# Performance work log

Measured on AMD Instinct MI355X. Metric: run time of the kernel, lower is better.

The kernel has to match this reference:

```python
import jax, jax.numpy as jnp
import numpy as np

C, G = 128, 2000          # num_cells, total_genes
CE, GE, H = 64, 64, 256   # cell_embed_dim, gene_embed_dim, hidden_dim
F = CE + GE + 3           # FCGNN input: ctrl val + cell_embed + gene_embed + shift + num_cells


def setup_inputs() -> dict:
    key = jax.random.key(0)
    ks = jax.random.split(key, 13)
    s = 0.02
    return {
        "ctrl": jax.random.uniform(ks[0], (C, G), dtype=jnp.float32),
        "shift_vec": jax.random.normal(ks[1], (G,), dtype=jnp.float32),
        "gene_indices": jnp.arange(G, dtype=jnp.int32),
        # CellEmbedding params
        "ce_w1": jax.random.normal(ks[2], (G, H), dtype=jnp.float32) * s,
        "ce_b1": jnp.zeros((H,), dtype=jnp.float32),
        "ce_w2": jax.random.normal(ks[3], (H, CE), dtype=jnp.float32) * s,
        "ce_b2": jnp.zeros((CE,), dtype=jnp.float32),
        # gene embedding table
        "gene_table": jax.random.normal(ks[4], (G, GE), dtype=jnp.float32) * s,
        # FCGNN params
        "g_w1": jax.random.normal(ks[5], (F, H), dtype=jnp.float32) * s,
        "g_b1": jnp.zeros((H,), dtype=jnp.float32),
        "g_w2": jax.random.normal(ks[6], (2 * H, H), dtype=jnp.float32) * s,
        "g_b2": jnp.zeros((H,), dtype=jnp.float32),
        "g_w3": jax.random.normal(ks[7], (2 * H, 1), dtype=jnp.float32) * s,
        "g_b3": jnp.zeros((1,), dtype=jnp.float32),
    }


def reference(ctrl, shift_vec, gene_indices, ce_w1, ce_b1, ce_w2, ce_b2,
              gene_table, g_w1, g_b1, g_w2, g_b2, g_w3, g_b3):
    num_cells = ctrl.shape[0]
    num_genes = gene_indices.shape[0]

    # CellEmbedding: fc2(elu(fc1(ctrl)))  -> [C, CE]
    ce = jax.nn.elu(ctrl @ ce_w1 + ce_b1) @ ce_w2 + ce_b2

    ctrl_g = ctrl[:, gene_indices]           # [C, Gn]
    shift = shift_vec[gene_indices]          # [Gn]
    ge = gene_table[gene_indices]            # [Gn, GE]

    # Build [C, Gn, F] feature tensor (ctrl val, cell embed, gene embed, shift, num_cells)
    z = jnp.concatenate([
        ctrl_g[:, :, None],
        jnp.broadcast_to(ce[:, None, :], (num_cells, num_genes, ce.shape[1])),
        jnp.broadcast_to(ge[None, :, :], (num_cells, num_genes, ge.shape[1])),
        jnp.broadcast_to(shift[None, :, None], (num_cells, num_genes, 1)),
        jnp.full((num_cells, num_genes, 1), float(num_cells), dtype=ctrl.dtype),
    ], axis=2)

    # FCGNN applied per gene (vectorized over gene axis); pooling is mean over cells (axis 0)
    x = jax.nn.elu(z @ g_w1 + g_b1)                                   # [C, Gn, H]
    p = x.mean(axis=0)                                                # [Gn, H]
    x = jnp.concatenate([x, jnp.broadcast_to(p[None], x.shape)], -1) @ g_w2 + g_b2
    p = x.mean(axis=0)
    x = jax.nn.elu(jnp.concatenate([x, jnp.broadcast_to(p[None], x.shape)], -1)) @ g_w3 + g_b3
    out = x[..., 0]                                                   # [C, Gn]

    # softmax over cells (torch Softmax(dim=0) after transpose/squeeze)
    return jax.nn.softmax(out, axis=0)
```

## Files before the change

kernel.cpp:

```cpp
#include <hip/hip_runtime.h>
#include <math.h>

#define G_GENES 2000
#define C_CELLS 128
#define H_DIM   256
#define CE_DIM  64
#define LDAe    264

typedef __attribute__((ext_vector_type(8))) short short8;
typedef __attribute__((ext_vector_type(4))) float floatx4;

__device__ __forceinline__ float eluf(float x) {
    float e = __expf(x) - 1.0f;
    return x > 0.0f ? x : e;
}
__device__ __forceinline__ unsigned short f2bf(float v) {
    unsigned u = __float_as_uint(v);
    u += 0x7FFF + ((u >> 16) & 1);
    return (unsigned short)(u >> 16);
}
__device__ __forceinline__ float bf2f(unsigned short s) {
    return __uint_as_float(((unsigned)s) << 16);
}

__global__ __launch_bounds__(256) void k1a(
    const float* __restrict__ ctrl, const float* __restrict__ ce_w1,
    float* __restrict__ hidpart)
{
    __shared__ float crow[250];
    const int c  = blockIdx.x >> 3;
    const int kc = blockIdx.x & 7;
    const int t  = threadIdx.x;

    if (t < 250) crow[t] = ctrl[(size_t)c * G_GENES + kc * 250 + t];
    __syncthreads();

    float s0 = 0.f, s1 = 0.f;
    const float* w = ce_w1 + (size_t)(kc * 250) * H_DIM + t;
    #pragma unroll 5
    for (int k = 0; k < 250; k += 2) {
        s0 = fmaf(crow[k], w[(size_t)k * H_DIM], s0);
        s1 = fmaf(crow[k + 1], w[(size_t)(k + 1) * H_DIM], s1);
    }
    hidpart[((size_t)c * 8 + kc) * H_DIM + t] = s0 + s1;
}

__global__ __launch_bounds__(256) void k1b(
    const float* __restrict__ hidpart, const float* __restrict__ ce_b1,
    const float* __restrict__ ce_w2, const float* __restrict__ ce_b2,
    const float* __restrict__ g_w1, float* __restrict__ Atc)
{
    __shared__ float hid[H_DIM];
    __shared__ float cel[CE_DIM];
    const int c = blockIdx.x;
    const int t = threadIdx.x;

    float s = ce_b1[t];
    #pragma unroll
    for (int p = 0; p < 8; ++p) s += hidpart[((size_t)c * 8 + p) * H_DIM + t];
    hid[t] = eluf(s);
    __syncthreads();

    if (t < CE_DIM) {
        float q = ce_b2[t];
        #pragma unroll 8
        for (int h = 0; h < H_DIM; ++h) q = fmaf(hid[h], ce_w2[(size_t)h * CE_DIM + t], q);
        cel[t] = q;
    }
    __syncthreads();

    float a = 0.f;
    #pragma unroll 8
    for (int e = 0; e < CE_DIM; ++e) a = fmaf(cel[e], g_w1[(size_t)(1 + e) * H_DIM + t], a);
    Atc[(size_t)c * H_DIM + t] = a;
}

__global__ __launch_bounds__(256) void k_w2abt(
    const float* __restrict__ g_w2, unsigned short* __restrict__ w2abt)
{
    const int n = blockIdx.x;
    const int k = threadIdx.x;
    w2abt[(size_t)n * H_DIM + k] = f2bf(g_w2[(size_t)k * H_DIM + n]);
}

__global__ __launch_bounds__(512, 4) void k_main(
    const float* __restrict__ ctrl, const float* __restrict__ shiftv,
    const int* __restrict__ gidx, const float* __restrict__ gtab,
    const float* __restrict__ g_w1, const float* __restrict__ g_b1,
    const float* __restrict__ g_w2, const float* __restrict__ g_b2,
    const float* __restrict__ g_w3, const float* __restrict__ Atc,
    const unsigned short* __restrict__ w2abt, float* __restrict__ out)
{
    __shared__ __align__(16) unsigned short x1t[C_CELLS * LDAe];
    __shared__ float cc[C_CELLS];
    __shared__ float gt[CE_DIM];
    __shared__ __align__(16) float Bv[H_DIM];
    __shared__ __align__(16) float w1r0[H_DIM];
    __shared__ float w3v[H_DIM];
    __shared__ float pvec[H_DIM];
    __shared__ float qv[H_DIM];
    __shared__ float red2[C_CELLS * 5];
    __shared__ float wred[4];

    const int g = blockIdx.x;
    const int t = threadIdx.x;
    const int idx = gidx[g];

    if (t < C_CELLS) cc[t] = ctrl[(size_t)t * G_GENES + idx];
    else if (t < C_CELLS + CE_DIM) gt[t - C_CELLS] = gtab[(size_t)idx * CE_DIM + (t - C_CELLS)];
    __syncthreads();

    if (t < H_DIM) {
        const float sh = shiftv[idx];
        float b = g_b1[t] + 128.0f * g_w1[(size_t)130 * H_DIM + t] + sh * g_w1[(size_t)129 * H_DIM + t];
        #pragma unroll 8
        for (int e = 0; e < CE_DIM; ++e) b = fmaf(gt[e], g_w1[(size_t)(65 + e) * H_DIM + t], b);
        Bv[t] = b;
        w1r0[t] = g_w1[t];
        w3v[t] = g_w3[t];
    }
    __syncthreads();

    {
        const int xc = t >> 2;
        const int xh = (t & 3) * 64;
        const float ccv = cc[xc];
        #pragma unroll
        for (int i = 0; i < 8; ++i) {
            const int h0 = xh + i * 8;
            float4 at0 = *(const float4*)(Atc + (size_t)xc * H_DIM + h0);
            float4 at1 = *(const float4*)(Atc + (size_t)xc * H_DIM + h0 + 4);
            float4 bv0 = *(const float4*)(Bv + h0);
            float4 bv1 = *(const float4*)(Bv + h0 + 4);
            float4 wr0 = *(const float4*)(w1r0 + h0);
            float4 wr1 = *(const float4*)(w1r0 + h0 + 4);
            float v0 = eluf(fmaf(ccv, wr0.x, at0.x + bv0.x));
            float v1 = eluf(fmaf(ccv, wr0.y, at0.y + bv0.y));
            float v2 = eluf(fmaf(ccv, wr0.z, at0.z + bv0.z));
            float v3 = eluf(fmaf(ccv, wr0.w, at0.w + bv0.w));
            float v4 = eluf(fmaf(ccv, wr1.x, at1.x + bv1.x));
            float v5 = eluf(fmaf(ccv, wr1.y, at1.y + bv1.y));
            float v6 = eluf(fmaf(ccv, wr1.z, at1.z + bv1.z));
            float v7 = eluf(fmaf(ccv, wr1.w, at1.w + bv1.w));
            uint4 pk;
            pk.x = (unsigned)f2bf(v0) | ((unsigned)f2bf(v1) << 16);
            pk.y = (unsigned)f2bf(v2) | ((unsigned)f2bf(v3) << 16);
            pk.z = (unsigned)f2bf(v4) | ((unsigned)f2bf(v5) << 16);
            pk.w = (unsigned)f2bf(v6) | ((unsigned)f2bf(v7) << 16);
            *(uint4*)&x1t[xc * LDAe + h0] = pk;
        }
    }
    __syncthreads();

    const int lane = t & 63;
    const int w    = t >> 6;
    const int quad = lane >> 4;
    const int nlo  = lane & 15;
    const int wm   = w >> 2;
    const int wn   = w & 3;

    {
        const int hh = w * 32 + (lane & 31);
        const int c0 = (lane >> 5) * 64;
        float s = 0.f;
        #pragma unroll 8
        for (int i = 0; i < 64; ++i) s += bf2f(x1t[(c0 + i) * LDAe + hh]);
        s += __shfl_xor(s, 32);
        if ((lane & 32) == 0) pvec[hh] = s * (1.0f / 128.0f);
    }
    __syncthreads();

    if (t < H_DIM) {
        float q = g_b2[t];
        const float* w2b = g_w2 + (size_t)H_DIM * H_DIM + t;
        #pragma unroll 8
        for (int h = 0; h < H_DIM; ++h) q = fmaf(pvec[h], w2b[(size_t)h * H_DIM], q);
        qv[t] = q;
    }

    floatx4 acc[4][4];
    #pragma unroll
    for (int mt = 0; mt < 4; ++mt)
        #pragma unroll
        for (int nt = 0; nt < 4; ++nt)
            acc[mt][nt] = (floatx4){0.f, 0.f, 0.f, 0.f};

    const unsigned short* bbase = w2abt + (size_t)(wn * 64 + nlo) * H_DIM + quad * 8;
    const unsigned short* abase = &x1t[(wm * 64 + nlo) * LDAe + quad * 8];

    for (int kt = 0; kt < 8; ++kt) {
        short8 af[4];
        #pragma unroll
        for (int mt = 0; mt < 4; ++mt)
            af[mt] = *(const short8*)(abase + mt * 16 * LDAe + kt * 32);
        #pragma unroll
        for (int nt = 0; nt < 4; ++nt) {
            short8 bf = *(const short8*)(bbase + (size_t)nt * 16 * H_DIM + kt * 32);
            #pragma unroll
            for (int mt = 0; mt < 4; ++mt)
                acc[mt][nt] = __builtin_amdgcn_mfma_f32_16x16x32_bf16(af[mt], bf, acc[mt][nt], 0, 0, 0);
        }
    }
    __syncthreads();

    float qj[4], w3j[4];
    #pragma unroll
    for (int nt = 0; nt < 4; ++nt) {
        const int j = wn * 64 + nt * 16 + nlo;
        qj[nt] = qv[j];
        w3j[nt] = w3v[j];
    }
    #pragma unroll
    for (int mt = 0; mt < 4; ++mt) {
        #pragma unroll
        for (int reg = 0; reg < 4; ++reg) {
            float part = 0.f;
            #pragma unroll
            for (int nt = 0; nt < 4; ++nt)
                part = fmaf(eluf(acc[mt][nt][reg] + qj[nt]), w3j[nt], part);
            part += __shfl_xor(part, 1);
            part += __shfl_xor(part, 2);
            part += __shfl_xor(part, 4);
            part += __shfl_xor(part, 8);
            if (nlo == 0)
                red2[(wm * 64 + mt * 16 + quad * 4 + reg) * 5 + wn] = part;
        }
    }
    __syncthreads();

    float s = 0.f, e = 0.f;
    if (t < C_CELLS) {
        s = red2[t * 5 + 0] + red2[t * 5 + 1] + red2[t * 5 + 2] + red2[t * 5 + 3];
        float m = s;
        #pragma unroll
        for (int off = 1; off < 64; off <<= 1) m = fmaxf(m, __shfl_xor(m, off));
        if (lane == 0) wred[w] = m;
    }
    __syncthreads();
    if (t < C_CELLS) {
        const float m = fmaxf(wred[0], wred[1]);
        e = __expf(s - m);
        float S = e;
        #pragma unroll
        for (int off = 1; off < 64; off <<= 1) S += __shfl_xor(S, off);
        if (lane == 0) wred[2 + w] = S;
    }
    __syncthreads();
    if (t < C_CELLS) out[(size_t)t * G_GENES + g] = e / (wred[2] + wred[3]);
}

extern "C" void kernel_launch(void* const* d_in, const int* in_sizes, int n_in,
                              void* d_out, int out_size, void* d_ws, size_t ws_size,
                              hipStream_t stream) {
    const float* ctrl   = (const float*)d_in[0];
    const float* shiftv = (const float*)d_in[1];
    const int*   gidx   = (const int*)d_in[2];
    const float* ce_w1  = (const float*)d_in[3];
    const float* ce_b1  = (const float*)d_in[4];
    const float* ce_w2  = (const float*)d_in[5];
    const float* ce_b2  = (const float*)d_in[6];
    const float* gtab   = (const float*)d_in[7];
    const float* g_w1   = (const float*)d_in[8];
    const float* g_b1   = (const float*)d_in[9];
    const float* g_w2   = (const float*)d_in[10];
    const float* g_b2   = (const float*)d_in[11];
    const float* g_w3   = (const float*)d_in[12];

    float* Atc = (float*)d_ws;
    unsigned short* w2abt = (unsigned short*)(Atc + C_CELLS * H_DIM);
    float* hidpart = (float*)(w2abt + H_DIM * H_DIM);
    float* out = (float*)d_out;

    k1a<<<C_CELLS * 8, 256, 0, stream>>>(ctrl, ce_w1, hidpart);
    k_w2abt<<<H_DIM, 256, 0, stream>>>(g_w2, w2abt);
    k1b<<<C_CELLS, 256, 0, stream>>>(hidpart, ce_b1, ce_w2, ce_b2, g_w1, Atc);
    k_main<<<G_GENES, 512, 0, stream>>>(ctrl, shiftv, gidx, gtab, g_w1, g_b1, g_w2, g_b2,
                                        g_w3, Atc, w2abt, out);
}
```

Baseline: 239.0 us.

## Split per-gene bias and pooled-projection into separate kernel before MFMA main kernel

Adds a new kernel k_pqb that computes, for each gene, the layer-1 bias vector, the cell-mean pooled vector (from fp32 elu values rather than bf16 x1t) and its projection through the second half of g_w2. It writes these to workspace, so the main MFMA kernel only loads them and no longer has serial reduction and GEMV phases or the extra barriers. It also splits k1a into 16 chunks and parallelises the ce_w2 GEMV in k1b across four partial sums. The cost is one extra launch and about 4 MB of extra global traffic, and hidpart now aliases the q_all buffer.

```diff
diff --git a/kernel.cpp b/kernel.cpp
--- a/kernel.cpp
+++ b/kernel.cpp
@@ -19,30 +19,24 @@
     u += 0x7FFF + ((u >> 16) & 1);
     return (unsigned short)(u >> 16);
 }
-__device__ __forceinline__ float bf2f(unsigned short s) {
-    return __uint_as_float(((unsigned)s) << 16);
-}
 
 __global__ __launch_bounds__(256) void k1a(
     const float* __restrict__ ctrl, const float* __restrict__ ce_w1,
     float* __restrict__ hidpart)
 {
-    __shared__ float crow[250];
-    const int c  = blockIdx.x >> 3;
-    const int kc = blockIdx.x & 7;
+    __shared__ float crow[125];
+    const int c  = blockIdx.x >> 4;
+    const int kc = blockIdx.x & 15;
     const int t  = threadIdx.x;
 
-    if (t < 250) crow[t] = ctrl[(size_t)c * G_GENES + kc * 250 + t];
-    __syncthreads();
-
-    float s0 = 0.f, s1 = 0.f;
-    const float* w = ce_w1 + (size_t)(kc * 250) * H_DIM + t;
+    if (t < 125) crow[t] = ctrl[(size_t)c * G_GENES + kc * 125 + t];
+    __syncthreads();
+
+    float s = 0.f;
+    const float* w = ce_w1 + (size_t)(kc * 125) * H_DIM + t;
     #pragma unroll 5
-    for (int k = 0; k < 250; k += 2) {
-        s0 = fmaf(crow[k], w[(size_t)k * H_DIM], s0);
-        s1 = fmaf(crow[k + 1], w[(size_t)(k + 1) * H_DIM], s1);
-    }
-    hidpart[((size_t)c * 8 + kc) * H_DIM + t] = s0 + s1;
+    for (int k = 0; k < 125; ++k) s = fmaf(crow[k], w[(size_t)k * H_DIM], s);
+    hidpart[((size_t)c * 16 + kc) * H_DIM + t] = s;
 }
 
 __global__ __launch_bounds__(256) void k1b(
@@ -51,22 +45,28 @@
     const float* __restrict__ g_w1, float* __restrict__ Atc)
 {
     __shared__ float hid[H_DIM];
+    __shared__ float celp[4 * CE_DIM];
     __shared__ float cel[CE_DIM];
     const int c = blockIdx.x;
     const int t = threadIdx.x;
 
     float s = ce_b1[t];
     #pragma unroll
-    for (int p = 0; p < 8; ++p) s += hidpart[((size_t)c * 8 + p) * H_DIM + t];
+    for (int p = 0; p < 16; ++p) s += hidpart[((size_t)c * 16 + p) * H_DIM + t];
     hid[t] = eluf(s);
     __syncthreads();
 
-    if (t < CE_DIM) {
-        float q = ce_b2[t];
+    {
+        const int e = t & 63, q4 = t >> 6;
+        float cp = 0.f;
+        const float* w2 = ce_w2 + (size_t)(q4 * 64) * CE_DIM + e;
         #pragma unroll 8
-        for (int h = 0; h < H_DIM; ++h) q = fmaf(hid[h], ce_w2[(size_t)h * CE_DIM + t], q);
-        cel[t] = q;
-    }
+        for (int h = 0; h < 64; ++h) cp = fmaf(hid[q4 * 64 + h], w2[(size_t)h * CE_DIM], cp);
+        celp[q4 * CE_DIM + e] = cp;
+    }
+    __syncthreads();
+    if (t < CE_DIM)
+        cel[t] = ce_b2[t] + celp[t] + celp[CE_DIM + t] + celp[2 * CE_DIM + t] + celp[3 * CE_DIM + t];
     __syncthreads();
 
     float a = 0.f;
@@ -83,24 +83,17 @@
     w2abt[(size_t)n * H_DIM + k] = f2bf(g_w2[(size_t)k * H_DIM + n]);
 }
 
-__global__ __launch_bounds__(512, 4) void k_main(
+__global__ __launch_bounds__(256) void k_pqb(
     const float* __restrict__ ctrl, const float* __restrict__ shiftv,
     const int* __restrict__ gidx, const float* __restrict__ gtab,
     const float* __restrict__ g_w1, const float* __restrict__ g_b1,
     const float* __restrict__ g_w2, const float* __restrict__ g_b2,
-    const float* __restrict__ g_w3, const float* __restrict__ Atc,
-    const unsigned short* __restrict__ w2abt, float* __restrict__ out)
-{
-    __shared__ __align__(16) unsigned short x1t[C_CELLS * LDAe];
+    const float* __restrict__ Atc, float* __restrict__ Bvg,
+    float* __restrict__ q_all)
+{
     __shared__ float cc[C_CELLS];
     __shared__ float gt[CE_DIM];
-    __shared__ __align__(16) float Bv[H_DIM];
-    __shared__ __align__(16) float w1r0[H_DIM];
-    __shared__ float w3v[H_DIM];
     __shared__ float pvec[H_DIM];
-    __shared__ float qv[H_DIM];
-    __shared__ float red2[C_CELLS * 5];
-    __shared__ float wred[4];
 
     const int g = blockIdx.x;
     const int t = threadIdx.x;
@@ -110,14 +103,55 @@
     else if (t < C_CELLS + CE_DIM) gt[t - C_CELLS] = gtab[(size_t)idx * CE_DIM + (t - C_CELLS)];
     __syncthreads();
 
+    const float w1r0 = g_w1[t];
+    float bv = g_b1[t] + 128.0f * g_w1[(size_t)130 * H_DIM + t]
+             + shiftv[idx] * g_w1[(size_t)129 * H_DIM + t];
+    #pragma unroll 8
+    for (int e = 0; e < CE_DIM; ++e) bv = fmaf(gt[e], g_w1[(size_t)(65 + e) * H_DIM + t], bv);
+    Bvg[(size_t)g * H_DIM + t] = bv;
+
+    float s = 0.f;
+    #pragma unroll 4
+    for (int c = 0; c < C_CELLS; ++c)
+        s += eluf(fmaf(cc[c], w1r0, Atc[(size_t)c * H_DIM + t] + bv));
+    pvec[t] = s * (1.0f / 128.0f);
+    __syncthreads();
+
+    float q = g_b2[t];
+    const float* w2b = g_w2 + (size_t)H_DIM * H_DIM + t;
+    #pragma unroll 8
+    for (int h = 0; h < H_DIM; ++h) q = fmaf(pvec[h], w2b[(size_t)h * H_DIM], q);
+    q_all[(size_t)g * H_DIM + t] = q;
+}
+
+__global__ __launch_bounds__(512, 4) void k_main(
+    const float* __restrict__ ctrl, const int* __restrict__ gidx,
+    const float* __restrict__ g_w1, const float* __restrict__ g_w3,
+    const float* __restrict__ Atc, const float* __restrict__ Bvg,
+    const float* __restrict__ q_all, const unsigned short* __restrict__ w2abt,
+    float* __restrict__ out)
+{
+    __shared__ __align__(16) unsigned short x1t[C_CELLS * LDAe];
+    __shared__ float cc[C_CELLS];
+    __shared__ float qv[H_DIM];
+    __shared__ float w3v[H_DIM];
+    __shared__ __align__(16) float Bvl[H_DIM];
+    __shared__ __align__(16) float w1l[H_DIM];
+    __shared__ float red2[C_CELLS * 5];
+    __shared__ float wred[4];
+
+    const int g = blockIdx.x;
+    const int t = threadIdx.x;
+    const int idx = gidx[g];
+
+    if (t < C_CELLS) cc[t] = ctrl[(size_t)t * G_GENES + idx];
     if (t < H_DIM) {
-        const float sh = shiftv[idx];
-        float b = g_b1[t] + 128.0f * g_w1[(size_t)130 * H_DIM + t] + sh * g_w1[(size_t)129 * H_DIM + t];
-        #pragma unroll 8
-        for (int e = 0; e < CE_DIM; ++e) b = fmaf(gt[e], g_w1[(size_t)(65 + e) * H_DIM + t], b);
-        Bv[t] = b;
-        w1r0[t] = g_w1[t];
+        qv[t]  = q_all[(size_t)g * H_DIM + t];
         w3v[t] = g_w3[t];
+    } else {
+        const int u = t - H_DIM;
+        Bvl[u] = Bvg[(size_t)g * H_DIM + u];
+        w1l[u] = g_w1[u];
     }
     __syncthreads();
 
@@ -130,10 +164,10 @@
             const int h0 = xh + i * 8;
             float4 at0 = *(const float4*)(Atc + (size_t)xc * H_DIM + h0);
             float4 at1 = *(const float4*)(Atc + (size_t)xc * H_DIM + h0 + 4);
-            float4 bv0 = *(const float4*)(Bv + h0);
-            float4 bv1 = *(const float4*)(Bv + h0 + 4);
-            float4 wr0 = *(const float4*)(w1r0 + h0);
-            float4 wr1 = *(const float4*)(w1r0 + h0 + 4);
+            float4 bv0 = *(const float4*)(Bvl + h0);
+            float4 bv1 = *(const float4*)(Bvl + h0 + 4);
+            float4 wr0 = *(const float4*)(w1l + h0);
+            float4 wr1 = *(const float4*)(w1l + h0 + 4);
             float v0 = eluf(fmaf(ccv, wr0.x, at0.x + bv0.x));
             float v1 = eluf(fmaf(ccv, wr0.y, at0.y + bv0.y));
             float v2 = eluf(fmaf(ccv, wr0.z, at0.z + bv0.z));
@@ -159,25 +193,6 @@
     const int wm   = w >> 2;
     const int wn   = w & 3;
 
-    {
-        const int hh = w * 32 + (lane & 31);
-        const int c0 = (lane >> 5) * 64;
-        float s = 0.f;
-        #pragma unroll 8
-        for (int i = 0; i < 64; ++i) s += bf2f(x1t[(c0 + i) * LDAe + hh]);
-        s += __shfl_xor(s, 32);
-        if ((lane & 32) == 0) pvec[hh] = s * (1.0f / 128.0f);
-    }
-    __syncthreads();
-
-    if (t < H_DIM) {
-        float q = g_b2[t];
-        const float* w2b = g_w2 + (size_t)H_DIM * H_DIM + t;
-        #pragma unroll 8
-        for (int h = 0; h < H_DIM; ++h) q = fmaf(pvec[h], w2b[(size_t)h * H_DIM], q);
-        qv[t] = q;
-    }
-
     floatx4 acc[4][4];
     #pragma unroll
     for (int mt = 0; mt < 4; ++mt)
@@ -201,7 +216,6 @@
                 acc[mt][nt] = __builtin_amdgcn_mfma_f32_16x16x32_bf16(af[mt], bf, acc[mt][nt], 0, 0, 0);
         }
     }
-    __syncthreads();
 
     float qj[4], w3j[4];
     #pragma unroll
@@ -266,14 +280,18 @@
     const float* g_b2   = (const float*)d_in[11];
     const float* g_w3   = (const float*)d_in[12];
 
-    float* Atc = (float*)d_ws;
-    unsigned short* w2abt = (unsigned short*)(Atc + C_CELLS * H_DIM);
-    float* hidpart = (float*)(w2abt + H_DIM * H_DIM);
-    float* out = (float*)d_out;
-
-    k1a<<<C_CELLS * 8, 256, 0, stream>>>(ctrl, ce_w1, hidpart);
+    char* ws = (char*)d_ws;
+    float* Atc            = (float*)(ws);
+    unsigned short* w2abt = (unsigned short*)(ws + 128 * 1024);
+    float* Bvg            = (float*)(ws + 256 * 1024);
+    float* q_all          = (float*)(ws + 256 * 1024 + (size_t)G_GENES * H_DIM * 4);
+    float* hidpart        = q_all;
+    float* out            = (float*)d_out;
+
+    k1a<<<C_CELLS * 16, 256, 0, stream>>>(ctrl, ce_w1, hidpart);
     k_w2abt<<<H_DIM, 256, 0, stream>>>(g_w2, w2abt);
     k1b<<<C_CELLS, 256, 0, stream>>>(hidpart, ce_b1, ce_w2, ce_b2, g_w1, Atc);
-    k_main<<<G_GENES, 512, 0, stream>>>(ctrl, shiftv, gidx, gtab, g_w1, g_b1, g_w2, g_b2,
-                                        g_w3, Atc, w2abt, out);
-}
+    k_pqb<<<G_GENES, 256, 0, stream>>>(ctrl, shiftv, gidx, gtab, g_w1, g_b1, g_w2, g_b2,
+                                       Atc, Bvg, q_all);
+    k_main<<<G_GENES, 512, 0, stream>>>(ctrl, gidx, g_w1, g_w3, Atc, Bvg, q_all, w2abt, out);
+}
```

Result: slower. 244.8 us (+2.4%).
